# Performance work log

Measured on AMD Instinct MI355X. Metric: run time of the kernel, lower is better.

The kernel has to match this reference:

```python
import jax, jax.numpy as jnp
import numpy as np

VOCAB = 50000; D = 512; H = 512; HD = H // 2; L = 2
T = 2048; NTAGS = 20; START = 18; END = 19
NEG = -10000.0


def setup_inputs() -> dict:
    key = jax.random.key(0)
    ks = jax.random.split(key, 24)
    s = 0.05
    rn = lambda k, shape: jax.random.normal(k, shape, jnp.float32) * s
    inp = {}
    inp["sentence"] = jax.random.randint(ks[0], (T,), 0, VOCAB)
    inp["emb"] = rn(ks[1], (VOCAB, D))
    i = 2
    for l in range(L):
        din = D if l == 0 else H
        for d in ("f", "b"):
            inp[f"l{l}{d}_Wih"] = rn(ks[i], (4 * HD, din)); i += 1
            inp[f"l{l}{d}_Whh"] = rn(ks[i], (4 * HD, HD)); i += 1
            inp[f"l{l}{d}_bih"] = rn(ks[i], (4 * HD,)); i += 1
            inp[f"l{l}{d}_bhh"] = rn(ks[i], (4 * HD,)); i += 1
    inp["W_out"] = rn(ks[i], (NTAGS, H)); i += 1
    inp["b_out"] = rn(ks[i], (NTAGS,)); i += 1
    tr = jax.random.normal(ks[i], (NTAGS, NTAGS), jnp.float32)
    tr = tr.at[START, :].set(NEG).at[:, END].set(NEG)
    inp["transitions"] = tr
    return inp


def _lstm_dir(x, Wih, Whh, bih, bhh, reverse):
    # x: [T, din]; precompute input contribution to all 4 gates (i,f,g,o order).
    xg = x @ Wih.T + bih  # [T, 4*HD]
    h0 = jnp.zeros((Whh.shape[1],), x.dtype)

    def step(carry, xt):
        h, c = carry
        z = xt + h @ Whh.T + bhh
        i, f, g, o = jnp.split(z, 4)
        c = jax.nn.sigmoid(f) * c + jax.nn.sigmoid(i) * jnp.tanh(g)
        h = jax.nn.sigmoid(o) * jnp.tanh(c)
        return (h, c), h

    _, hs = jax.lax.scan(step, (h0, h0), xg, reverse=reverse)
    return hs  # [T, HD], outputs aligned with timesteps in both directions


def _feats(sentence, emb, layers, W_out, b_out):
    x = emb[sentence]  # [T, D]
    for (Wf, Uf, bf, cf, Wb, Ub, bb, cb) in layers:
        hf = _lstm_dir(x, Wf, Uf, bf, cf, False)
        hb = _lstm_dir(x, Wb, Ub, bb, cb, True)
        x = jnp.concatenate([hf, hb], axis=-1)  # [T, H]
    return x @ W_out.T + b_out  # [T, NTAGS]


def _viterbi(feats, transitions):
    v0 = jnp.full((NTAGS,), NEG, feats.dtype).at[START].set(0.0)

    def step(v, feat):
        scores = v[None, :] + transitions  # [next_tag, prev_tag]
        bp = jnp.argmax(scores, axis=1)
        v_new = jnp.max(scores, axis=1) + feat
        return v_new, bp

    v_last, bps = jax.lax.scan(step, v0, feats)  # bps: [T, NTAGS]
    terminal = v_last + transitions[END]
    best = jnp.argmax(terminal)
    score = terminal[best]

    def back(tag, bp):
        return bp[tag], tag  # emit tag at this timestep, move to its predecessor

    _, path = jax.lax.scan(back, best, bps, reverse=True)
    return score, path


def reference(sentence, emb, l0f_Wih, l0f_Whh, l0f_bih, l0f_bhh, l0b_Wih, l0b_Whh, l0b_bih, l0b_bhh, l1f_Wih, l1f_Whh, l1f_bih, l1f_bhh, l1b_Wih, l1b_Whh, l1b_bih, l1b_bhh, W_out, b_out, transitions):
    layers = [
        (l0f_Wih, l0f_Whh, l0f_bih, l0f_bhh, l0b_Wih, l0b_Whh, l0b_bih, l0b_bhh),
        (l1f_Wih, l1f_Whh, l1f_bih, l1f_bhh, l1b_Wih, l1b_Whh, l1b_bih, l1b_bhh),
    ]
    feats = _feats(sentence, emb, layers, W_out, b_out)
    return _viterbi(feats, transitions)
```

## Files before the change

### kernel.cpp

```cpp
#include <hip/hip_runtime.h>
#include <math.h>


#define T_LEN 2048
#define DMODEL 512
#define HD 256
#define NTAGS 20
#define START_TAG 18
#define END_TAG 19

__device__ __forceinline__ float fsig(float x) {
  return 1.0f / (1.0f + __expf(-x));
}
__device__ __forceinline__ float ftanh(float x) {
  float xc = fminf(15.0f, fmaxf(-15.0f, x));
  float e = __expf(2.0f * xc);
  return (e - 1.0f) / (e + 1.0f);
}

__global__ void embed_k(const int* __restrict__ sent,
                        const float* __restrict__ emb,
                        float* __restrict__ x0) {
  int t = blockIdx.x;
  int tid = threadIdx.x;
  int tok = sent[t];
  const float4* src = (const float4*)(emb + (size_t)tok * DMODEL);
  float4* dst = (float4*)(x0 + (size_t)t * DMODEL);
  dst[tid] = src[tid];
}

__global__ __launch_bounds__(256) void gemm_xg_k(
    const float* __restrict__ X,
    const float* __restrict__ Wf, const float* __restrict__ Wb,
    const float* __restrict__ bf, const float* __restrict__ bb,
    float* __restrict__ outf, float* __restrict__ outb) {
  int bx = blockIdx.x;
  int by = blockIdx.y;
  int dir = blockIdx.z;
  const float* W = dir ? Wb : Wf;
  const float* bias = dir ? bb : bf;
  float* out = dir ? outb : outf;

  __shared__ __align__(16) float Xs[16][132];
  __shared__ __align__(16) float Ws[16][132];

  int tid = threadIdx.x;
  int tx = tid & 15;
  int ty = tid >> 4;

  float acc[8][8];
#pragma unroll
  for (int i = 0; i < 8; i++)
#pragma unroll
    for (int j = 0; j < 8; j++) acc[i][j] = 0.0f;

  for (int kt = 0; kt < DMODEL / 16; kt++) {
    __syncthreads();
#pragma unroll
    for (int l = 0; l < 2; l++) {
      int fi = tid + l * 256;
      int row = fi >> 2;
      int kq = fi & 3;
      float4 xv = *(const float4*)(X + (size_t)(by * 128 + row) * DMODEL + kt * 16 + kq * 4);
      Xs[kq * 4 + 0][row] = xv.x;
      Xs[kq * 4 + 1][row] = xv.y;
      Xs[kq * 4 + 2][row] = xv.z;
      Xs[kq * 4 + 3][row] = xv.w;
      float4 wv = *(const float4*)(W + (size_t)(bx * 128 + row) * DMODEL + kt * 16 + kq * 4);
      Ws[kq * 4 + 0][row] = wv.x;
      Ws[kq * 4 + 1][row] = wv.y;
      Ws[kq * 4 + 2][row] = wv.z;
      Ws[kq * 4 + 3][row] = wv.w;
    }
    __syncthreads();
#pragma unroll
    for (int k = 0; k < 16; k++) {
      float4 a0 = *(const float4*)&Xs[k][ty * 4];
      float4 a1 = *(const float4*)&Xs[k][64 + ty * 4];
      float4 b0 = *(const float4*)&Ws[k][tx * 4];
      float4 b1 = *(const float4*)&Ws[k][64 + tx * 4];
      float a[8] = {a0.x, a0.y, a0.z, a0.w, a1.x, a1.y, a1.z, a1.w};
      float b[8] = {b0.x, b0.y, b0.z, b0.w, b1.x, b1.y, b1.z, b1.w};
#pragma unroll
      for (int i = 0; i < 8; i++)
#pragma unroll
        for (int j = 0; j < 8; j++) acc[i][j] += a[i] * b[j];
    }
  }

  float4 bv0 = *(const float4*)(bias + bx * 128 + tx * 4);
  float4 bv1 = *(const float4*)(bias + bx * 128 + 64 + tx * 4);
  float bb8[8] = {bv0.x, bv0.y, bv0.z, bv0.w, bv1.x, bv1.y, bv1.z, bv1.w};
#pragma unroll
  for (int i = 0; i < 8; i++) {
    int row = by * 128 + ((i < 4) ? (ty * 4 + i) : (64 + ty * 4 + (i - 4)));
    float4 o0 = {acc[i][0] + bb8[0], acc[i][1] + bb8[1], acc[i][2] + bb8[2], acc[i][3] + bb8[3]};
    float4 o1 = {acc[i][4] + bb8[4], acc[i][5] + bb8[5], acc[i][6] + bb8[6], acc[i][7] + bb8[7]};
    *(float4*)(out + (size_t)row * 1024 + bx * 128 + tx * 4) = o0;
    *(float4*)(out + (size_t)row * 1024 + bx * 128 + 64 + tx * 4) = o1;
  }
}

__global__ __launch_bounds__(256) void recur_k(
    const float* __restrict__ xg_f, const float* __restrict__ xg_b,
    const float* __restrict__ Whh_f, const float* __restrict__ Whh_b,
    const float* __restrict__ bhh_f, const float* __restrict__ bhh_b,
    float* __restrict__ xnext, unsigned long long* __restrict__ hcomm_base) {
  int kc = blockIdx.x;
  int dir = blockIdx.y;
  int tid = threadIdx.x;

  const float* Whh = dir ? Whh_b : Whh_f;
  const float* bhh = dir ? bhh_b : bhh_f;
  const float* xg = dir ? xg_b : xg_f;
  unsigned long long* hcomm = hcomm_base + (size_t)dir * 2 * HD;

  int r = tid >> 1;
  int half = tid & 1;
  int g = r >> 5;
  int kl = r & 31;
  int grow = g * 256 + kc * 32 + kl;

  float4 Wv[32];
  const float4* wrow = (const float4*)(Whh + (size_t)grow * HD + half * 128);
#pragma unroll
  for (int j = 0; j < 32; j++) Wv[j] = wrow[j];
  float bias = bhh[grow];

  __shared__ __align__(16) float hbuf[HD];
  __shared__ float zbuf[128];
  hbuf[tid] = 0.0f;
  __syncthreads();

  float c = 0.0f;
  bool is_remote = ((tid >> 5) != kc);

#pragma unroll 1
  for (int it = 0; it < T_LEN; ++it) {
    int t = dir ? (T_LEN - 1 - it) : it;
    int p = it & 1;
    unsigned int tag = (unsigned)(it + 1);

    float xgv = 0.0f;
    if (!half) xgv = xg[(size_t)t * 1024 + grow];

    const float4* h4 = (const float4*)hbuf + half * 32;
    float4 acc = {0.f, 0.f, 0.f, 0.f};
#pragma unroll
    for (int j = 0; j < 32; j++) {
      float4 hv = h4[j];
      acc.x += Wv[j].x * hv.x;
      acc.y += Wv[j].y * hv.y;
      acc.z += Wv[j].z * hv.z;
      acc.w += Wv[j].w * hv.w;
    }
    float s = (acc.x + acc.y) + (acc.z + acc.w);
    s += __shfl_xor(s, 1, 64);
    if (!half) zbuf[r] = s + xgv + bias;
    __syncthreads();

    if (tid < 32) {
      float zi = zbuf[tid];
      float zf = zbuf[32 + tid];
      float zg = zbuf[64 + tid];
      float zo = zbuf[96 + tid];
      c = fsig(zf) * c + fsig(zi) * ftanh(zg);
      float h = fsig(zo) * ftanh(c);
      xnext[(size_t)t * DMODEL + dir * HD + kc * 32 + tid] = h;
      hbuf[kc * 32 + tid] = h;
      union { float f; unsigned u; } cv;
      cv.f = h;
      __hip_atomic_store(&hcomm[p * HD + kc * 32 + tid],
                         ((unsigned long long)tag << 32) | cv.u,
                         __ATOMIC_RELAXED, __HIP_MEMORY_SCOPE_AGENT);
    }
    if (is_remote) {
      unsigned long long v;
      do {
        v = __hip_atomic_load(&hcomm[p * HD + tid], __ATOMIC_RELAXED,
                              __HIP_MEMORY_SCOPE_AGENT);
      } while ((unsigned)(v >> 32) != tag);
      union { unsigned u; float f; } cv;
      cv.u = (unsigned)v;
      hbuf[tid] = cv.f;
    }
    __syncthreads();
  }
}

__global__ void proj_k(const float* __restrict__ x2,
                       const float* __restrict__ Wo,
                       const float* __restrict__ bo,
                       float* __restrict__ feats) {
  int t = blockIdx.x;
  int tid = threadIdx.x;
  int n = tid & 31;
  int seg = tid >> 5;
  __shared__ float red[8][32];
  float s = 0.0f;
  if (n < NTAGS) {
    const float* xr = x2 + (size_t)t * DMODEL + seg * 64;
    const float* wr = Wo + (size_t)n * DMODEL + seg * 64;
#pragma unroll
    for (int j = 0; j < 64; j++) s += xr[j] * wr[j];
  }
  red[seg][n] = s;
  __syncthreads();
  if (tid < NTAGS) {
    float tot = bo[tid];
#pragma unroll
    for (int k = 0; k < 8; k++) tot += red[k][tid];
    feats[(size_t)t * NTAGS + tid] = tot;
  }
}

__global__ void viterbi_k(const float* __restrict__ feats,
                          const float* __restrict__ tr,
                          float* __restrict__ out) {
  __shared__ float v[NTAGS];
  __shared__ unsigned char bp[T_LEN * NTAGS];
  __shared__ float term[NTAGS];
  int tid = threadIdx.x;

  float trrow[NTAGS];
  if (tid < NTAGS) {
#pragma unroll
    for (int p = 0; p < NTAGS; p++) trrow[p] = tr[tid * NTAGS + p];
    v[tid] = (tid == START_TAG) ? 0.0f : -10000.0f;
  }
  __syncthreads();

#pragma unroll 1
  for (int t = 0; t < T_LEN; t++) {
    float fv = 0.0f;
    if (tid < NTAGS) fv = feats[(size_t)t * NTAGS + tid];
    float best = -3.4e38f;
    int arg = 0;
    if (tid < NTAGS) {
#pragma unroll
      for (int p = 0; p < NTAGS; p++) {
        float sc = v[p] + trrow[p];
        if (sc > best) { best = sc; arg = p; }
      }
      bp[t * NTAGS + tid] = (unsigned char)arg;
    }
    __syncthreads();
    if (tid < NTAGS) v[tid] = best + fv;
    __syncthreads();
  }

  if (tid < NTAGS) term[tid] = v[tid] + tr[END_TAG * NTAGS + tid];
  __syncthreads();
  if (tid == 0) {
    float bs = term[0];
    int bi = 0;
    for (int p = 1; p < NTAGS; p++) {
      if (term[p] > bs) { bs = term[p]; bi = p; }
    }
    out[0] = bs;
    int tag = bi;
    for (int t = T_LEN - 1; t >= 0; t--) {
      out[1 + t] = (float)tag;
      tag = bp[t * NTAGS + tag];
    }
  }
}

extern "C" void kernel_launch(void* const* d_in, const int* in_sizes, int n_in,
                              void* d_out, int out_size, void* d_ws, size_t ws_size,
                              hipStream_t stream) {
  const int* sent = (const int*)d_in[0];
  const float* emb = (const float*)d_in[1];
  const float* l0f_Wih = (const float*)d_in[2];
  const float* l0f_Whh = (const float*)d_in[3];
  const float* l0f_bih = (const float*)d_in[4];
  const float* l0f_bhh = (const float*)d_in[5];
  const float* l0b_Wih = (const float*)d_in[6];
  const float* l0b_Whh = (const float*)d_in[7];
  const float* l0b_bih = (const float*)d_in[8];
  const float* l0b_bhh = (const float*)d_in[9];
  const float* l1f_Wih = (const float*)d_in[10];
  const float* l1f_Whh = (const float*)d_in[11];
  const float* l1f_bih = (const float*)d_in[12];
  const float* l1f_bhh = (const float*)d_in[13];
  const float* l1b_Wih = (const float*)d_in[14];
  const float* l1b_Whh = (const float*)d_in[15];
  const float* l1b_bih = (const float*)d_in[16];
  const float* l1b_bhh = (const float*)d_in[17];
  const float* W_out = (const float*)d_in[18];
  const float* b_out = (const float*)d_in[19];
  const float* transitions = (const float*)d_in[20];

  char* ws = (char*)d_ws;
  size_t off = 0;
  float* x0 = (float*)(ws + off);  off += (size_t)T_LEN * DMODEL * 4;
  float* xgf = (float*)(ws + off); off += (size_t)T_LEN * 1024 * 4;
  float* xgb = (float*)(ws + off); off += (size_t)T_LEN * 1024 * 4;
  float* x1 = (float*)(ws + off);  off += (size_t)T_LEN * DMODEL * 4;
  float* x2 = (float*)(ws + off);  off += (size_t)T_LEN * DMODEL * 4;
  float* feats = (float*)(ws + off); off += (size_t)T_LEN * NTAGS * 4;
  off = (off + 127) & ~(size_t)127;
  unsigned long long* hcomm0 = (unsigned long long*)(ws + off);
  off += (size_t)2 * 2 * HD * 8;
  unsigned long long* hcomm1 = (unsigned long long*)(ws + off);
  off += (size_t)2 * 2 * HD * 8;

  float* outf = (float*)d_out;

  (void)hipMemsetAsync(hcomm0, 0, (size_t)2 * 2 * 2 * HD * 8, stream);

  embed_k<<<dim3(T_LEN), dim3(128), 0, stream>>>(sent, emb, x0);

  gemm_xg_k<<<dim3(8, 16, 2), dim3(256), 0, stream>>>(
      x0, l0f_Wih, l0b_Wih, l0f_bih, l0b_bih, xgf, xgb);

  recur_k<<<dim3(8, 2), dim3(256), 0, stream>>>(
      xgf, xgb, l0f_Whh, l0b_Whh, l0f_bhh, l0b_bhh, x1, hcomm0);

  gemm_xg_k<<<dim3(8, 16, 2), dim3(256), 0, stream>>>(
      x1, l1f_Wih, l1b_Wih, l1f_bih, l1b_bih, xgf, xgb);

  recur_k<<<dim3(8, 2), dim3(256), 0, stream>>>(
      xgf, xgb, l1f_Whh, l1b_Whh, l1f_bhh, l1b_bhh, x2, hcomm1);

  proj_k<<<dim3(T_LEN), dim3(256), 0, stream>>>(x2, W_out, b_out, feats);

  viterbi_k<<<dim3(1), dim3(64), 0, stream>>>(feats, transitions, outf);
}
```

Before: 8.036 ms.

## Co-locate recurrence blocks on one XCD and exchange hidden state via L2

The recurrence kernel now launches 128 candidate blocks per direction. Each block reads its XCC_ID and joins an election, so that eight blocks on the same XCD do the work and the rest exit. When co-location succeeds, the blocks check that L2-level publish and read work between them. If it does, they exchange per-step hidden state with volatile stores and sc0 atomic reads that stay in the shared XCD L2, avoiding device-scope coherence traffic across XCDs. This adds election overhead and depends on undocumented block-placement behaviour, with a fallback to the old atomic path.

```diff
diff --git a/kernel.cpp b/kernel.cpp
--- a/kernel.cpp
+++ b/kernel.cpp
@@ -8,6 +8,7 @@
 #define NTAGS 20
 #define START_TAG 18
 #define END_TAG 19
+#define NCAND 128
 
 __device__ __forceinline__ float fsig(float x) {
   return 1.0f / (1.0f + __expf(-x));
@@ -16,6 +17,20 @@
   float xc = fminf(15.0f, fmaxf(-15.0f, x));
   float e = __expf(2.0f * xc);
   return (e - 1.0f) / (e + 1.0f);
+}
+
+__device__ __forceinline__ unsigned long long rd_l2(unsigned long long* p) {
+  unsigned long long old;
+  unsigned long long zero = 0;
+  asm volatile("global_atomic_add_x2 %0, %1, %2, off sc0\n\ts_waitcnt vmcnt(0)"
+               : "=&v"(old)
+               : "v"(p), "v"(zero)
+               : "memory");
+  return old;
+}
+__device__ __forceinline__ void pub_l2(unsigned long long* p,
+                                       unsigned long long v) {
+  *(volatile unsigned long long*)p = v;
 }
 
 __global__ void embed_k(const int* __restrict__ sent,
@@ -105,10 +120,103 @@
     const float* __restrict__ xg_f, const float* __restrict__ xg_b,
     const float* __restrict__ Whh_f, const float* __restrict__ Whh_b,
     const float* __restrict__ bhh_f, const float* __restrict__ bhh_b,
-    float* __restrict__ xnext, unsigned long long* __restrict__ hcomm_base) {
-  int kc = blockIdx.x;
+    float* __restrict__ xnext, unsigned long long* __restrict__ hcomm_base,
+    int* __restrict__ elect_base, unsigned long long* __restrict__ probe_base,
+    int* __restrict__ vote_base) {
   int dir = blockIdx.y;
   int tid = threadIdx.x;
+
+  int xcd;
+  asm volatile("s_getreg_b32 %0, hwreg(HW_REG_XCC_ID)" : "=s"(xcd));
+  xcd &= 7;
+  int* cnt = elect_base + dir * (1 + NCAND);
+  int* tab = cnt + 1;
+
+  __shared__ int e_tab[NCAND];
+  __shared__ int e_info[4];
+  __shared__ int probe_ok[8];
+  if (tid == 0) {
+    int ticket = __hip_atomic_fetch_add(cnt, 1, __ATOMIC_RELAXED,
+                                        __HIP_MEMORY_SCOPE_AGENT);
+    __hip_atomic_store(&tab[ticket], xcd + 1, __ATOMIC_RELAXED,
+                       __HIP_MEMORY_SCOPE_AGENT);
+    e_info[0] = ticket;
+  }
+  if (tid < NCAND) {
+    int v;
+    do {
+      v = __hip_atomic_load(&tab[tid], __ATOMIC_RELAXED,
+                            __HIP_MEMORY_SCOPE_AGENT);
+    } while (v == 0);
+    e_tab[tid] = v - 1;
+  }
+  __syncthreads();
+  if (tid == 0) {
+    int ticket = e_info[0];
+    int counts[8] = {0, 0, 0, 0, 0, 0, 0, 0};
+    int home = -1;
+    for (int i = 0; i < NCAND; i++) {
+      int x = e_tab[i];
+      counts[x]++;
+      if (counts[x] == 8 && home < 0) home = x;
+    }
+    int sel = 0, kc = 0, probe = 0;
+    if (home >= 0) {
+      if (xcd == home) {
+        int rank = 0;
+        for (int i = 0; i < ticket; i++)
+          if (e_tab[i] == home) rank++;
+        if (rank < 8) { sel = 1; kc = rank; probe = 1; }
+      }
+    } else {
+      if (ticket < 8) { sel = 1; kc = ticket; probe = 0; }
+    }
+    e_info[1] = sel; e_info[2] = kc; e_info[3] = probe;
+  }
+  __syncthreads();
+  if (!e_info[1]) return;
+  int kc = e_info[2];
+  int do_probe = e_info[3];
+  int use_l2 = 0;
+
+  if (do_probe) {
+    unsigned long long* probe = probe_base + (size_t)dir * 8 * 16;
+    int* vote = vote_base + dir * 8;
+    if (tid == 0) {
+      pub_l2(&probe[kc * 16], 0xBEEF000000000000ull + (unsigned)kc);
+    }
+    if (tid < 8) {
+      int found = 0;
+      for (int iter = 0; iter < 3000 && !found; ++iter) {
+        if (rd_l2(&probe[tid * 16]) ==
+            0xBEEF000000000000ull + (unsigned)tid) found = 1;
+      }
+      probe_ok[tid] = found;
+    }
+    __syncthreads();
+    if (tid == 0) {
+      int ok = 1;
+      for (int i = 0; i < 8; i++) ok &= probe_ok[i];
+      __hip_atomic_store(&vote[kc], 1 + ok, __ATOMIC_RELAXED,
+                         __HIP_MEMORY_SCOPE_AGENT);
+    }
+    if (tid < 8) {
+      int v;
+      do {
+        v = __hip_atomic_load(&vote[tid], __ATOMIC_RELAXED,
+                              __HIP_MEMORY_SCOPE_AGENT);
+      } while (v == 0);
+      probe_ok[tid] = v;
+    }
+    __syncthreads();
+    if (tid == 0) {
+      int all2 = 1;
+      for (int i = 0; i < 8; i++) all2 &= (probe_ok[i] == 2);
+      e_info[3] = all2;
+    }
+    __syncthreads();
+    use_l2 = e_info[3];
+  }
 
   const float* Whh = dir ? Whh_b : Whh_f;
   const float* bhh = dir ? bhh_b : bhh_f;
@@ -166,20 +274,28 @@
       float zo = zbuf[96 + tid];
       c = fsig(zf) * c + fsig(zi) * ftanh(zg);
       float h = fsig(zo) * ftanh(c);
+      union { float f; unsigned u; } cv;
+      cv.f = h;
+      unsigned long long pkt = ((unsigned long long)tag << 32) | cv.u;
+      if (use_l2) {
+        pub_l2(&hcomm[p * HD + kc * 32 + tid], pkt);
+      } else {
+        __hip_atomic_store(&hcomm[p * HD + kc * 32 + tid], pkt,
+                           __ATOMIC_RELAXED, __HIP_MEMORY_SCOPE_AGENT);
+      }
       xnext[(size_t)t * DMODEL + dir * HD + kc * 32 + tid] = h;
       hbuf[kc * 32 + tid] = h;
-      union { float f; unsigned u; } cv;
-      cv.f = h;
-      __hip_atomic_store(&hcomm[p * HD + kc * 32 + tid],
-                         ((unsigned long long)tag << 32) | cv.u,
-                         __ATOMIC_RELAXED, __HIP_MEMORY_SCOPE_AGENT);
     }
     if (is_remote) {
       unsigned long long v;
-      do {
-        v = __hip_atomic_load(&hcomm[p * HD + tid], __ATOMIC_RELAXED,
-                              __HIP_MEMORY_SCOPE_AGENT);
-      } while ((unsigned)(v >> 32) != tag);
+      if (use_l2) {
+        do { v = rd_l2(&hcomm[p * HD + tid]); } while ((unsigned)(v >> 32) != tag);
+      } else {
+        do {
+          v = __hip_atomic_load(&hcomm[p * HD + tid], __ATOMIC_RELAXED,
+                                __HIP_MEMORY_SCOPE_AGENT);
+        } while ((unsigned)(v >> 32) != tag);
+      }
       union { unsigned u; float f; } cv;
       cv.u = (unsigned)v;
       hbuf[tid] = cv.f;
@@ -299,29 +415,39 @@
   float* x1 = (float*)(ws + off);  off += (size_t)T_LEN * DMODEL * 4;
   float* x2 = (float*)(ws + off);  off += (size_t)T_LEN * DMODEL * 4;
   float* feats = (float*)(ws + off); off += (size_t)T_LEN * NTAGS * 4;
+
   off = (off + 127) & ~(size_t)127;
-  unsigned long long* hcomm0 = (unsigned long long*)(ws + off);
-  off += (size_t)2 * 2 * HD * 8;
-  unsigned long long* hcomm1 = (unsigned long long*)(ws + off);
-  off += (size_t)2 * 2 * HD * 8;
+  char* sync_area = ws + off;
+  unsigned long long* hcomm0 = (unsigned long long*)(sync_area);
+  unsigned long long* hcomm1 = (unsigned long long*)(sync_area + 8192);
+  int* elect0 = (int*)(sync_area + 16384);
+  int* elect1 = (int*)(sync_area + 18432);
+  unsigned long long* probe0 = (unsigned long long*)(sync_area + 20480);
+  unsigned long long* probe1 = (unsigned long long*)(sync_area + 22528);
+  int* vote0 = (int*)(sync_area + 24576);
+  int* vote1 = (int*)(sync_area + 25600);
+  size_t sync_bytes = 26624;
+  off += sync_bytes;
 
   float* outf = (float*)d_out;
 
-  (void)hipMemsetAsync(hcomm0, 0, (size_t)2 * 2 * 2 * HD * 8, stream);
+  (void)hipMemsetAsync(sync_area, 0, sync_bytes, stream);
 
   embed_k<<<dim3(T_LEN), dim3(128), 0, stream>>>(sent, emb, x0);
 
   gemm_xg_k<<<dim3(8, 16, 2), dim3(256), 0, stream>>>(
       x0, l0f_Wih, l0b_Wih, l0f_bih, l0b_bih, xgf, xgb);
 
-  recur_k<<<dim3(8, 2), dim3(256), 0, stream>>>(
-      xgf, xgb, l0f_Whh, l0b_Whh, l0f_bhh, l0b_bhh, x1, hcomm0);
+  recur_k<<<dim3(NCAND, 2), dim3(256), 0, stream>>>(
+      xgf, xgb, l0f_Whh, l0b_Whh, l0f_bhh, l0b_bhh, x1, hcomm0, elect0,
+      probe0, vote0);
 
   gemm_xg_k<<<dim3(8, 16, 2), dim3(256), 0, stream>>>(
       x1, l1f_Wih, l1b_Wih, l1f_bih, l1b_bih, xgf, xgb);
 
-  recur_k<<<dim3(8, 2), dim3(256), 0, stream>>>(
-      xgf, xgb, l1f_Whh, l1b_Whh, l1f_bhh, l1b_bhh, x2, hcomm1);
+  recur_k<<<dim3(NCAND, 2), dim3(256), 0, stream>>>(
+      xgf, xgb, l1f_Whh, l1b_Whh, l1f_bhh, l1b_bhh, x2, hcomm1, elect1,
+      probe1, vote1);
 
   proj_k<<<dim3(T_LEN), dim3(256), 0, stream>>>(x2, W_out, b_out, feats);
 
```

Result: no change. 8.027 ms (-0.1%).
